# Kernel tuning notes

Hardware: AMD Instinct MI355X
Metric: run time of the kernel (lower is better)

The kernel has to match this reference:

```python
import jax, jax.numpy as jnp
import numpy as np

PART_INDICES = [[0, 1, 2, 3, 4], [5, 6, 11, 12], [5, 7, 9], [6, 8, 10], [11, 12, 13, 14, 15, 16]]
B, J, D_IN, D_H, D_OUT = 4096, 25, 512, 256, 512


def _xavier(key, shape):
    fan_in, fan_out = shape
    lim = float(np.sqrt(6.0 / (fan_in + fan_out)))
    return jax.random.uniform(key, shape, jnp.float32, -lim, lim)


def setup_inputs() -> dict:
    key = jax.random.key(0)
    ks = list(jax.random.split(key, 64))
    it = iter(ks)
    inp = {}
    inp["x"] = jax.random.normal(next(it), (B, J, D_IN), jnp.float32)
    inp["adj_global"] = jax.random.uniform(next(it), (J, J), jnp.float32)
    for p, idx in enumerate(PART_INDICES):
        n = len(idx)
        inp[f"adj_local_{p}"] = jax.random.uniform(next(it), (n, n), jnp.float32)
    # global GCN params (2 layers)
    inp["Wg0"] = _xavier(next(it), (D_IN, D_H)); inp["bg0"] = jnp.zeros((D_H,), jnp.float32)
    inp["Wg1"] = _xavier(next(it), (D_H, D_OUT)); inp["bg1"] = jnp.zeros((D_OUT,), jnp.float32)
    # local GCN params (5 parts x 2 layers)
    for p in range(5):
        inp[f"Wl{p}a"] = _xavier(next(it), (D_IN, D_H)); inp[f"bl{p}a"] = jnp.zeros((D_H,), jnp.float32)
        inp[f"Wl{p}b"] = _xavier(next(it), (D_H, D_OUT)); inp[f"bl{p}b"] = jnp.zeros((D_OUT,), jnp.float32)
    # fusion MLP: Linear(2*D_OUT, D_OUT) -> ReLU -> Linear(D_OUT, D_OUT)
    inp["Wf0"] = _xavier(next(it), (2 * D_OUT, D_OUT)); inp["bf0"] = jnp.zeros((D_OUT,), jnp.float32)
    inp["Wf1"] = _xavier(next(it), (D_OUT, D_OUT)); inp["bf1"] = jnp.zeros((D_OUT,), jnp.float32)
    return inp


def _gcn(x, adj, W, b):
    # symmetric degree normalization D^-1/2 A D^-1/2, then (norm_adj @ (x @ W)) + b
    d = jnp.clip(adj.sum(axis=1), 1e-6, None) ** -0.5
    norm_adj = d[:, None] * adj * d[None, :]                       # [n, n]
    return jnp.einsum('ij,bjf->bif', norm_adj, x @ W) + b          # [B, n, out]


def reference(x, adj_global, adj_local_0, adj_local_1, adj_local_2, adj_local_3, adj_local_4,
              Wg0, bg0, Wg1, bg1,
              Wl0a, bl0a, Wl0b, bl0b,
              Wl1a, bl1a, Wl1b, bl1b,
              Wl2a, bl2a, Wl2b, bl2b,
              Wl3a, bl3a, Wl3b, bl3b,
              Wl4a, bl4a, Wl4b, bl4b,
              Wf0, bf0, Wf1, bf1):
    adjs = [adj_local_0, adj_local_1, adj_local_2, adj_local_3, adj_local_4]
    lps = [(Wl0a, bl0a, Wl0b, bl0b), (Wl1a, bl1a, Wl1b, bl1b), (Wl2a, bl2a, Wl2b, bl2b),
           (Wl3a, bl3a, Wl3b, bl3b), (Wl4a, bl4a, Wl4b, bl4b)]
    # global branch
    xg = jax.nn.relu(_gcn(x, adj_global, Wg0, bg0))
    xg = jax.nn.relu(_gcn(xg, adj_global, Wg1, bg1))
    # local branch: scatter per-part outputs back (later parts overwrite overlaps, like torch)
    xl = jnp.zeros((x.shape[0], x.shape[1], D_OUT), x.dtype)
    for p, idx in enumerate(PART_INDICES):
        Wa, ba, Wb, bb = lps[p]
        idx_a = jnp.asarray(idx)
        xp = x[:, idx_a]                                           # [B, n_p, D_IN]
        xp = jax.nn.relu(_gcn(xp, adjs[p], Wa, ba))
        xp = jax.nn.relu(_gcn(xp, adjs[p], Wb, bb))
        xl = xl.at[:, idx_a].set(xp)
    # fusion MLP
    xc = jnp.concatenate([xg, xl], axis=-1)                        # [B, J, 2*D_OUT]
    return jax.nn.relu(xc @ Wf0 + bf0) @ Wf1 + bf1                 # [B, J, D_OUT]
```

## Files before the change

kernel.cpp:

```cpp
#include <hip/hip_runtime.h>


#define BATCH 4096
#define NJOINT 25
#define MROWS (BATCH * NJOINT)
#define SZ_FULL (MROWS * 512)

typedef __attribute__((ext_vector_type(8))) short short8;
typedef __attribute__((ext_vector_type(4))) float float4_;

__device__ __forceinline__ float b2f(ushort u) {
    union { float f; uint32_t i; } x; x.i = ((uint32_t)u) << 16; return x.f;
}
__device__ __forceinline__ ushort f2b(float f) {
    union { float f; uint32_t i; } x; x.f = f;
    uint32_t r = x.i + 0x7fff + ((x.i >> 16) & 1);
    return (ushort)(r >> 16);
}
__device__ __forceinline__ void async16(const void* g, void* l) {
    __builtin_amdgcn_global_load_lds(
        (const __attribute__((address_space(1))) void*)g,
        (__attribute__((address_space(3))) void*)l, 16, 0, 0);
}

__device__ void norm_one(const float* A, int n, float* out, float* sAdj, float* sD) {
    int t = threadIdx.x;
    for (int i = t; i < n * n; i += 256) sAdj[i] = A[i];
    __syncthreads();
    if (t < n) {
        float s = 0.f;
        for (int j = 0; j < n; j++) s += sAdj[t * n + j];
        sD[t] = 1.0f / sqrtf(fmaxf(s, 1e-6f));
    }
    __syncthreads();
    for (int i = t; i < n * n; i += 256) {
        int r = i / n, c = i % n;
        out[i] = sD[r] * sAdj[i] * sD[c];
    }
    __syncthreads();
}

__global__ __launch_bounds__(256) void adjnorm_kernel(
    const float* Ag, const float* A0, const float* A2, const float* A3,
    const float* A4, float* ADJ) {
    __shared__ float sAdj[640];
    __shared__ float sD[32];
    norm_one(Ag, 25, ADJ, sAdj, sD);
    norm_one(A0, 5, ADJ + 640 + 0 * 64, sAdj, sD);
    norm_one(A2, 3, ADJ + 640 + 1 * 64, sAdj, sD);
    norm_one(A3, 3, ADJ + 640 + 2 * 64, sAdj, sD);
    norm_one(A4, 6, ADJ + 640 + 3 * 64, sAdj, sD);
}

__global__ __launch_bounds__(256) void cvt_bf16(const float* __restrict__ in,
                                                ushort* __restrict__ out, int n4) {
    int id = blockIdx.x * 256 + threadIdx.x;
    if (id < n4) {
        float4 v = ((const float4*)in)[id];
        ushort4 o;
        o.x = f2b(v.x); o.y = f2b(v.y); o.z = f2b(v.z); o.w = f2b(v.w);
        ((ushort4*)out)[id] = o;
    }
}

__global__ __launch_bounds__(256) void wtrans(const float* __restrict__ W,
                                              ushort* __restrict__ Wt, int K, int N) {
    __shared__ float tile[32][33];
    int t = threadIdx.x;
    int tx = t & 31, ty = t >> 5;
    int k0 = blockIdx.y * 32, n0 = blockIdx.x * 32;
    for (int r = ty; r < 32; r += 8)
        tile[r][tx] = W[(size_t)(k0 + r) * N + n0 + tx];
    __syncthreads();
    for (int r = ty; r < 32; r += 8)
        Wt[(size_t)(n0 + r) * K + k0 + tx] = f2b(tile[tx][r]);
}

__global__ __launch_bounds__(256) void zero_tail(ushort* __restrict__ XGL) {
    int id = blockIdx.x * 256 + threadIdx.x;
    int f4 = id & 127;
    int rj = (id >> 7) & 7;
    int b = id >> 10;
    ushort4 z; z.x = 0; z.y = 0; z.z = 0; z.w = 0;
    ((ushort4*)(XGL + ((size_t)(b * 25 + 17 + rj) * 1024 + 512)))[f4] = z;
}

template <bool GATHER, bool BIAS, bool RELU, bool OUTF32>
__global__ __launch_bounds__(512, 2) void gemm256(
    const ushort* __restrict__ A, const ushort* __restrict__ Wt,
    const float* __restrict__ bias, void* __restrict__ C,
    int M, int N, int K, int lda, int ldc,
    int gn, int g0, int g1, int g2, int g3, int g4, int g5) {
    __shared__ ushort lds[65536];
    int t = threadIdx.x;
    int l = t & 63, w = t >> 6;

    int nwg = (int)gridDim.x;
    int cpx = nwg >> 3;
    int wg = ((int)blockIdx.x & 7) * cpx + ((int)blockIdx.x >> 3);
    int gx = N >> 8;
    int tm = wg / gx, tn = wg - tm * gx;
    int bm = tm << 8, bn = tn << 8;

    int rA0 = (w << 4) + (l >> 2);
    int rA1 = 128 + rA0;
    int qp = l & 3;
    int qA0 = qp ^ ((rA0 >> 1) & 3);
    int qA1 = qp ^ ((rA1 >> 1) & 3);
    int grA0 = bm + rA0, grA1 = bm + rA1;
    if (GATHER) {
        int map[6] = {g0, g1, g2, g3, g4, g5};
        int b0 = grA0 / gn; grA0 = b0 * 25 + map[grA0 - b0 * gn];
        int b1 = grA1 / gn; grA1 = b1 * 25 + map[grA1 - b1 * gn];
    }
    const ushort* pA0 = A + (size_t)grA0 * lda + (qA0 << 3);
    const ushort* pA1 = A + (size_t)grA1 * lda + (qA1 << 3);
    const ushort* pB0 = Wt + (size_t)(bn + rA0) * K + (qA0 << 3);
    const ushort* pB1 = Wt + (size_t)(bn + rA1) * K + (qA1 << 3);
    int sA0 = w << 9;
    int sA1 = (8 + w) << 9;

    int wm = w >> 2, wn = w & 3;
    int lr = l & 15, q = l >> 4;
    int aoff[8], boff[4];
#pragma unroll
    for (int fi = 0; fi < 8; fi++) {
        int r = (wm << 7) + (fi << 4) + lr;
        aoff[fi] = (r << 5) + ((q ^ ((r >> 1) & 3)) << 3);
    }
#pragma unroll
    for (int fj = 0; fj < 4; fj++) {
        int r = (wn << 6) + (fj << 4) + lr;
        boff[fj] = 8192 + (r << 5) + ((q ^ ((r >> 1) & 3)) << 3);
    }

    float4_ acc[8][4];
#pragma unroll
    for (int fi = 0; fi < 8; fi++)
#pragma unroll
        for (int fj = 0; fj < 4; fj++) acc[fi][fj] = (float4_)0.f;

    int NT = K >> 5;

#define STAGE(kt_) do {                                      \
        int bo_ = ((kt_) & 3) << 14;                         \
        int ko_ = (kt_) << 5;                                \
        async16(pA0 + ko_, &lds[bo_ + sA0]);                 \
        async16(pA1 + ko_, &lds[bo_ + sA1]);                 \
        async16(pB0 + ko_, &lds[bo_ + 8192 + sA0]);          \
        async16(pB1 + ko_, &lds[bo_ + 8192 + sA1]);          \
    } while (0)

    STAGE(0);
    STAGE(1);
    for (int kt = 0; kt < NT; ++kt) {
        if (kt + 2 < NT) {
            STAGE(kt + 2);
            asm volatile("s_waitcnt vmcnt(8)" ::: "memory");
        } else if (kt + 1 < NT) {
            asm volatile("s_waitcnt vmcnt(4)" ::: "memory");
        } else {
            asm volatile("s_waitcnt vmcnt(0)" ::: "memory");
        }
        __builtin_amdgcn_s_barrier();
        __builtin_amdgcn_sched_barrier(0);
        int bo = (kt & 3) << 14;
        short8 af[8], bf[4];
#pragma unroll
        for (int fj = 0; fj < 4; fj++) bf[fj] = *(const short8*)&lds[bo + boff[fj]];
#pragma unroll
        for (int fi = 0; fi < 8; fi++) af[fi] = *(const short8*)&lds[bo + aoff[fi]];
        __builtin_amdgcn_s_setprio(1);
#pragma unroll
        for (int fi = 0; fi < 8; fi++)
#pragma unroll
            for (int fj = 0; fj < 4; fj++)
                acc[fi][fj] = __builtin_amdgcn_mfma_f32_16x16x32_bf16(
                    af[fi], bf[fj], acc[fi][fj], 0, 0, 0);
        __builtin_amdgcn_s_setprio(0);
    }
#undef STAGE

    int cl = lr;
    float bv[4];
#pragma unroll
    for (int fj = 0; fj < 4; fj++)
        bv[fj] = BIAS ? bias[bn + (wn << 6) + (fj << 4) + cl] : 0.f;
#pragma unroll
    for (int fi = 0; fi < 8; fi++) {
        int row0 = bm + (wm << 7) + (fi << 4) + (q << 2);
#pragma unroll
        for (int r = 0; r < 4; r++) {
            size_t rowoff = (size_t)(row0 + r) * ldc;
#pragma unroll
            for (int fj = 0; fj < 4; fj++) {
                int col = bn + (wn << 6) + (fj << 4) + cl;
                float v = acc[fi][fj][r] + bv[fj];
                if (RELU) v = fmaxf(v, 0.f);
                if (OUTF32)
                    ((float*)C)[rowoff + col] = v;
                else
                    ((ushort*)C)[rowoff + col] = f2b(v);
            }
        }
    }
    (void)M;
}

template <int NJ>
__global__ __launch_bounds__(256) void mix_inplace(
    ushort* __restrict__ T, const float* __restrict__ adjn,
    const float* __restrict__ bias, int F, int ldr) {
    __shared__ float As[NJ * NJ];
    int t = threadIdx.x;
    for (int i = t; i < NJ * NJ; i += 256) As[i] = adjn[i];
    __syncthreads();
    int id = blockIdx.x * 256 + t;
    int f = id % F;
    int b = id / F;
    ushort* base = T + (size_t)(b * NJ) * ldr + f;
    float v[NJ];
#pragma unroll
    for (int j = 0; j < NJ; j++) v[j] = b2f(base[(size_t)j * ldr]);
    float bi = bias[f];
#pragma unroll
    for (int i = 0; i < NJ; i++) {
        float o = 0.f;
#pragma unroll
        for (int j = 0; j < NJ; j++) o += As[i * NJ + j] * v[j];
        base[(size_t)i * ldr] = f2b(fmaxf(o + bi, 0.f));
    }
}

template <int NJ>
__global__ __launch_bounds__(256) void mix_scatter(
    const ushort* __restrict__ P, const float* __restrict__ adjn,
    const float* __restrict__ bias, ushort* __restrict__ XL,
    int j0, int j1, int j2, int j3, int j4, int j5) {
    __shared__ float As[NJ * NJ];
    __shared__ int jm[NJ];
    int t = threadIdx.x;
    for (int i = t; i < NJ * NJ; i += 256) As[i] = adjn[i];
    if (t == 0) {
        int tmp[6] = {j0, j1, j2, j3, j4, j5};
        for (int i = 0; i < NJ; i++) jm[i] = tmp[i];
    }
    __syncthreads();
    int id = blockIdx.x * 256 + t;
    int f = id & 511;
    int b = id >> 9;
    float v[NJ];
    const ushort* base = P + (size_t)(b * NJ) * 512 + f;
#pragma unroll
    for (int j = 0; j < NJ; j++) v[j] = b2f(base[(size_t)j * 512]);
    float bi = bias[f];
#pragma unroll
    for (int i = 0; i < NJ; i++) {
        float o = 0.f;
#pragma unroll
        for (int j = 0; j < NJ; j++) o += As[i * NJ + j] * v[j];
        XL[((size_t)(b * 25 + jm[i])) * 1024 + f] = f2b(fmaxf(o + bi, 0.f));
    }
}

extern "C" void kernel_launch(void* const* d_in, const int* in_sizes, int n_in,
                              void* d_out, int out_size, void* d_ws,
                              size_t ws_size, hipStream_t stream) {
    const float* x    = (const float*)d_in[0];
    const float* adjg = (const float*)d_in[1];
    const float* al0  = (const float*)d_in[2];
    const float* al2  = (const float*)d_in[4];
    const float* al3  = (const float*)d_in[5];
    const float* al4  = (const float*)d_in[6];
    const float* Wg0  = (const float*)d_in[7];
    const float* bg0  = (const float*)d_in[8];
    const float* Wg1  = (const float*)d_in[9];
    const float* bg1  = (const float*)d_in[10];
    const float* Wf0  = (const float*)d_in[31];
    const float* bf0  = (const float*)d_in[32];
    const float* Wf1  = (const float*)d_in[33];
    const float* bf1  = (const float*)d_in[34];

    float* ws = (float*)d_ws;
    float* ADJ = ws;
    ushort* U  = (ushort*)(ws + 4096);
    ushort* Xb  = U;
    ushort* XGL = U + (size_t)SZ_FULL;
    ushort* S   = XGL + (size_t)MROWS * 1024;
    ushort* T  = S;
    ushort* P1 = S;
    ushort* P3 = S + 6291456;
    ushort* Wb = S + 26214400;
    ushort* HF = Xb;

    ushort* Wg0t = Wb;
    ushort* Wg1t = Wb + 131072;
    ushort* Wf0t = Wb + 1310720;
    ushort* Wf1t = Wb + 1835008;

    dim3 blk(256);
    dim3 blk512(512);

    adjnorm_kernel<<<1, blk, 0, stream>>>(adjg, al0, al2, al3, al4, ADJ);
    cvt_bf16<<<SZ_FULL / 4 / 256, blk, 0, stream>>>(x, Xb, SZ_FULL / 4);
    zero_tail<<<16384, blk, 0, stream>>>(XGL);

    wtrans<<<dim3(256 / 32, 512 / 32), blk, 0, stream>>>(Wg0, Wg0t, 512, 256);
    wtrans<<<dim3(512 / 32, 256 / 32), blk, 0, stream>>>(Wg1, Wg1t, 256, 512);
    wtrans<<<dim3(512 / 32, 1024 / 32), blk, 0, stream>>>(Wf0, Wf0t, 1024, 512);
    wtrans<<<dim3(512 / 32, 512 / 32), blk, 0, stream>>>(Wf1, Wf1t, 512, 512);

    struct Part { int n, widx; int idx[6]; };
    const Part parts[4] = {
        {5, 11, {0, 1, 2, 3, 4, 0}},
        {3, 19, {5, 7, 9, 0, 0, 0}},
        {3, 23, {6, 8, 10, 0, 0, 0}},
        {6, 27, {11, 12, 13, 14, 15, 16}},
    };
    for (int q = 0; q < 4; q++) {
        ushort* Wat = Wb + 262144 + q * 262144;
        ushort* Wbt = Wat + 131072;
        wtrans<<<dim3(8, 16), blk, 0, stream>>>((const float*)d_in[parts[q].widx], Wat, 512, 256);
        wtrans<<<dim3(16, 8), blk, 0, stream>>>((const float*)d_in[parts[q].widx + 2], Wbt, 256, 512);
    }

    gemm256<false, false, false, false><<<400, blk512, 0, stream>>>(
        Xb, Wg0t, nullptr, T, MROWS, 256, 512, 512, 256, 0, 0, 0, 0, 0, 0, 0);
    mix_inplace<25><<<BATCH * 256 / 256, blk, 0, stream>>>(T, ADJ, bg0, 256, 256);
    gemm256<false, false, false, false><<<800, blk512, 0, stream>>>(
        T, Wg1t, nullptr, XGL, MROWS, 512, 256, 256, 1024, 0, 0, 0, 0, 0, 0, 0);
    mix_inplace<25><<<BATCH * 512 / 256, blk, 0, stream>>>(XGL, ADJ, bg1, 512, 1024);

    const int slots[4] = {0, 1, 2, 3};
    for (int q = 0; q < 4; q++) {
        const Part& P = parts[q];
        const float* ba = (const float*)d_in[P.widx + 1];
        const float* bb = (const float*)d_in[P.widx + 3];
        ushort* Wat = Wb + 262144 + q * 262144;
        ushort* Wbt = Wat + 131072;
        const float* adjl = ADJ + 640 + slots[q] * 64;
        int M = BATCH * P.n;
        gemm256<true, false, false, false><<<M / 256, blk512, 0, stream>>>(
            Xb, Wat, nullptr, P1, M, 256, 512, 512, 256,
            P.n, P.idx[0], P.idx[1], P.idx[2], P.idx[3], P.idx[4], P.idx[5]);
        if (P.n == 5)
            mix_inplace<5><<<BATCH * 256 / 256, blk, 0, stream>>>(P1, adjl, ba, 256, 256);
        else if (P.n == 3)
            mix_inplace<3><<<BATCH * 256 / 256, blk, 0, stream>>>(P1, adjl, ba, 256, 256);
        else
            mix_inplace<6><<<BATCH * 256 / 256, blk, 0, stream>>>(P1, adjl, ba, 256, 256);
        gemm256<false, false, false, false><<<(M / 256) * 2, blk512, 0, stream>>>(
            P1, Wbt, nullptr, P3, M, 512, 256, 256, 512, 0, 0, 0, 0, 0, 0, 0);
        if (P.n == 5)
            mix_scatter<5><<<BATCH * 512 / 256, blk, 0, stream>>>(
                P3, adjl, bb, XGL + 512, P.idx[0], P.idx[1], P.idx[2], P.idx[3], P.idx[4], P.idx[5]);
        else if (P.n == 3)
            mix_scatter<3><<<BATCH * 512 / 256, blk, 0, stream>>>(
                P3, adjl, bb, XGL + 512, P.idx[0], P.idx[1], P.idx[2], P.idx[3], P.idx[4], P.idx[5]);
        else
            mix_scatter<6><<<BATCH * 512 / 256, blk, 0, stream>>>(
                P3, adjl, bb, XGL + 512, P.idx[0], P.idx[1], P.idx[2], P.idx[3], P.idx[4], P.idx[5]);
    }

    gemm256<false, true, true, false><<<800, blk512, 0, stream>>>(
        XGL, Wf0t, bf0, HF, MROWS, 512, 1024, 1024, 512, 0, 0, 0, 0, 0, 0, 0);
    gemm256<false, true, false, true><<<800, blk512, 0, stream>>>(
        HF, Wf1t, bf1, (float*)d_out, MROWS, 512, 512, 512, 512, 0, 0, 0, 0, 0, 0, 0);

    (void)in_sizes; (void)n_in; (void)out_size; (void)ws_size;
}
```

Baseline: 1.055 ms.

## Restructure GEMM mainloop into 8-phase ping-pong with 64-wide K tiles

Rewrites the gemm256 main loop to use K tiles of 64 with two LDS buffers. Each K tile is split into four phases of two A fragments each, and the async global-to-LDS loads for the next tile are interleaved into those phases. The LDS layout and XOR swizzle change to fit 64-element rows, and B fragments are held in registers for the whole tile. The aim is finer-grained overlap of loads, LDS reads and MFMA work, at the cost of more barriers per tile and tricky vmcnt bookkeeping that must stay correct when K/64 is even.

```diff
diff --git a/kernel.cpp b/kernel.cpp
--- a/kernel.cpp
+++ b/kernel.cpp
@@ -102,84 +102,116 @@
     int tm = wg / gx, tn = wg - tm * gx;
     int bm = tm << 8, bn = tn << 8;
 
-    int rA0 = (w << 4) + (l >> 2);
-    int rA1 = 128 + rA0;
-    int qp = l & 3;
-    int qA0 = qp ^ ((rA0 >> 1) & 3);
-    int qA1 = qp ^ ((rA1 >> 1) & 3);
-    int grA0 = bm + rA0, grA1 = bm + rA1;
-    if (GATHER) {
-        int map[6] = {g0, g1, g2, g3, g4, g5};
-        int b0 = grA0 / gn; grA0 = b0 * 25 + map[grA0 - b0 * gn];
-        int b1 = grA1 / gn; grA1 = b1 * 25 + map[grA1 - b1 * gn];
-    }
-    const ushort* pA0 = A + (size_t)grA0 * lda + (qA0 << 3);
-    const ushort* pA1 = A + (size_t)grA1 * lda + (qA1 << 3);
-    const ushort* pB0 = Wt + (size_t)(bn + rA0) * K + (qA0 << 3);
-    const ushort* pB1 = Wt + (size_t)(bn + rA1) * K + (qA1 << 3);
-    int sA0 = w << 9;
-    int sA1 = (8 + w) << 9;
+    int srow = (w << 4) + (l >> 3);
+    int sch = ((l & 7) ^ (l >> 3)) << 3;
+    const ushort* pA[2][2];
+    const ushort* pB[2][2];
+    {
+        int map_[6] = {g0, g1, g2, g3, g4, g5};
+#pragma unroll
+        for (int h = 0; h < 2; h++)
+#pragma unroll
+            for (int i = 0; i < 2; i++) {
+                int r = bm + h * 128 + srow + i * 8;
+                if (GATHER) { int b = r / gn; r = b * 25 + map_[r - b * gn]; }
+                pA[h][i] = A + (size_t)r * lda + sch;
+                int c = bn + h * 128 + srow + i * 8;
+                pB[h][i] = Wt + (size_t)c * K + sch;
+            }
+    }
+    int stga = w << 10;
 
     int wm = w >> 2, wn = w & 3;
     int lr = l & 15, q = l >> 4;
-    int aoff[8], boff[4];
-#pragma unroll
-    for (int fi = 0; fi < 8; fi++) {
-        int r = (wm << 7) + (fi << 4) + lr;
-        aoff[fi] = (r << 5) + ((q ^ ((r >> 1) & 3)) << 3);
-    }
-#pragma unroll
-    for (int fj = 0; fj < 4; fj++) {
-        int r = (wn << 6) + (fj << 4) + lr;
-        boff[fj] = 8192 + (r << 5) + ((q ^ ((r >> 1) & 3)) << 3);
-    }
+    int cx = lr & 7;
+    int ca0 = (q ^ cx) << 3;
+    int ca1 = ca0 ^ 32;
+    int ra = (wm << 13) + (lr << 6);
+    int rb = 16384 + ((wn >> 1) << 13) + ((wn & 1) << 12) + (lr << 6);
 
     float4_ acc[8][4];
 #pragma unroll
     for (int fi = 0; fi < 8; fi++)
 #pragma unroll
         for (int fj = 0; fj < 4; fj++) acc[fi][fj] = (float4_)0.f;
-
-    int NT = K >> 5;
-
-#define STAGE(kt_) do {                                      \
-        int bo_ = ((kt_) & 3) << 14;                         \
-        int ko_ = (kt_) << 5;                                \
-        async16(pA0 + ko_, &lds[bo_ + sA0]);                 \
-        async16(pA1 + ko_, &lds[bo_ + sA1]);                 \
-        async16(pB0 + ko_, &lds[bo_ + 8192 + sA0]);          \
-        async16(pB1 + ko_, &lds[bo_ + 8192 + sA1]);          \
+    short8 bfr[4][2];
+
+#define STG_A(DB, H, KT) do {                                              \
+        async16(pA[H][0] + (KT) * 64, &lds[(DB) + (H) * 8192 + stga]);     \
+        async16(pA[H][1] + (KT) * 64, &lds[(DB) + (H) * 8192 + stga + 512]); \
     } while (0)
-
-    STAGE(0);
-    STAGE(1);
-    for (int kt = 0; kt < NT; ++kt) {
-        if (kt + 2 < NT) {
-            STAGE(kt + 2);
-            asm volatile("s_waitcnt vmcnt(8)" ::: "memory");
-        } else if (kt + 1 < NT) {
-            asm volatile("s_waitcnt vmcnt(4)" ::: "memory");
-        } else {
-            asm volatile("s_waitcnt vmcnt(0)" ::: "memory");
-        }
-        __builtin_amdgcn_s_barrier();
-        __builtin_amdgcn_sched_barrier(0);
-        int bo = (kt & 3) << 14;
-        short8 af[8], bf[4];
-#pragma unroll
-        for (int fj = 0; fj < 4; fj++) bf[fj] = *(const short8*)&lds[bo + boff[fj]];
-#pragma unroll
-        for (int fi = 0; fi < 8; fi++) af[fi] = *(const short8*)&lds[bo + aoff[fi]];
-        __builtin_amdgcn_s_setprio(1);
-#pragma unroll
-        for (int fi = 0; fi < 8; fi++)
-#pragma unroll
-            for (int fj = 0; fj < 4; fj++)
-                acc[fi][fj] = __builtin_amdgcn_mfma_f32_16x16x32_bf16(
-                    af[fi], bf[fj], acc[fi][fj], 0, 0, 0);
-        __builtin_amdgcn_s_setprio(0);
-    }
-#undef STAGE
+#define STG_B(DB, H, KT) do {                                              \
+        async16(pB[H][0] + (KT) * 64, &lds[(DB) + 16384 + (H) * 8192 + stga]); \
+        async16(pB[H][1] + (KT) * 64, &lds[(DB) + 16384 + (H) * 8192 + stga + 512]); \
+    } while (0)
+
+#define DO_PHASE(DB, FI0, RDB, WAITST, ...) do {                           \
+        short8 af00, af01, af10, af11;                                     \
+        if (RDB) {                                                         \
+            _Pragma("unroll")                                              \
+            for (int fj = 0; fj < 4; fj++) {                               \
+                bfr[fj][0] = *(const short8*)&lds[(DB) + rb + fj * 1024 + ca0]; \
+                bfr[fj][1] = *(const short8*)&lds[(DB) + rb + fj * 1024 + ca1]; \
+            }                                                              \
+        }                                                                  \
+        af00 = *(const short8*)&lds[(DB) + ra + (FI0) * 1024 + ca0];       \
+        af01 = *(const short8*)&lds[(DB) + ra + (FI0) * 1024 + ca1];       \
+        af10 = *(const short8*)&lds[(DB) + ra + ((FI0) + 1) * 1024 + ca0]; \
+        af11 = *(const short8*)&lds[(DB) + ra + ((FI0) + 1) * 1024 + ca1]; \
+        __VA_ARGS__                                                        \
+        WAITST                                                             \
+        if (RDB) asm volatile("s_waitcnt lgkmcnt(8)");                     \
+        __builtin_amdgcn_sched_barrier(0);                                 \
+        __builtin_amdgcn_s_barrier();                                      \
+        asm volatile("s_waitcnt lgkmcnt(0)" ::: "memory");                 \
+        __builtin_amdgcn_sched_barrier(0);                                 \
+        __builtin_amdgcn_s_setprio(1);                                     \
+        _Pragma("unroll")                                                  \
+        for (int fj = 0; fj < 4; fj++) {                                   \
+            acc[FI0][fj] = __builtin_amdgcn_mfma_f32_16x16x32_bf16(        \
+                af00, bfr[fj][0], acc[FI0][fj], 0, 0, 0);                  \
+            acc[FI0][fj] = __builtin_amdgcn_mfma_f32_16x16x32_bf16(        \
+                af01, bfr[fj][1], acc[FI0][fj], 0, 0, 0);                  \
+            acc[(FI0) + 1][fj] = __builtin_amdgcn_mfma_f32_16x16x32_bf16(  \
+                af10, bfr[fj][0], acc[(FI0) + 1][fj], 0, 0, 0);            \
+            acc[(FI0) + 1][fj] = __builtin_amdgcn_mfma_f32_16x16x32_bf16(  \
+                af11, bfr[fj][1], acc[(FI0) + 1][fj], 0, 0, 0);            \
+        }                                                                  \
+        __builtin_amdgcn_s_setprio(0);                                     \
+        __builtin_amdgcn_sched_barrier(0);                                 \
+        __builtin_amdgcn_s_barrier();                                      \
+    } while (0)
+
+    int NT = K >> 6;
+    int NITER = NT >> 1;
+
+    STG_A(0, 0, 0); STG_A(0, 1, 0);
+    STG_B(0, 0, 0); STG_B(0, 1, 0);
+    STG_B(32768, 0, 1); STG_B(32768, 1, 1);
+    asm volatile("s_waitcnt vmcnt(4)" ::: "memory");
+    __builtin_amdgcn_sched_barrier(0);
+    __builtin_amdgcn_s_barrier();
+
+    for (int j = 0; j < NITER; ++j) {
+        int k1 = 2 * j + 1, k2 = 2 * j + 2, k3 = 2 * j + 3;
+        bool nl = (j + 1 < NITER);
+        DO_PHASE(0, 0, true, , STG_A(32768, 0, k1););
+        DO_PHASE(0, 2, false, , STG_A(32768, 1, k1););
+        DO_PHASE(0, 4, false, , if (nl) STG_B(0, 0, k2););
+        DO_PHASE(0, 6, false,
+                 if (nl) { asm volatile("s_waitcnt vmcnt(4)" ::: "memory"); }
+                 else    { asm volatile("s_waitcnt vmcnt(0)" ::: "memory"); },
+                 if (nl) STG_B(0, 1, k2););
+        DO_PHASE(32768, 0, true, , if (nl) STG_A(0, 0, k2););
+        DO_PHASE(32768, 2, false, , if (nl) STG_A(0, 1, k2););
+        DO_PHASE(32768, 4, false, , if (nl) STG_B(32768, 0, k3););
+        DO_PHASE(32768, 6, false,
+                 if (nl) { asm volatile("s_waitcnt vmcnt(4)" ::: "memory"); },
+                 if (nl) STG_B(32768, 1, k3););
+    }
+#undef DO_PHASE
+#undef STG_A
+#undef STG_B
 
     int cl = lr;
     float bv[4];
```

Result: faster. 1.031 ms (-2.3%).
